# Optimization experiments

Measured on AMD Instinct MI355X. Metric: run time of the kernel, lower is better.

## Reference

```python
import jax, jax.numpy as jnp
import numpy as np

D = 768
H = 12
W = 128
HD = D // H
EPS = 1e-5


def setup_inputs() -> dict:
    key = jax.random.key(0)
    ks = jax.random.split(key, 10)
    B, L = 4, 8190
    s = 1.0 / np.sqrt(D)
    inp = {
        "expanded": jax.random.normal(ks[0], (B, L, D), dtype=jnp.float32),
        "Wq": jax.random.normal(ks[1], (D, D), dtype=jnp.float32) * s,
        "bq": jnp.zeros((D,), jnp.float32),
        "Wk": jax.random.normal(ks[2], (D, D), dtype=jnp.float32) * s,
        "bk": jnp.zeros((D,), jnp.float32),
        "Wv": jax.random.normal(ks[3], (D, D), dtype=jnp.float32) * s,
        "bv": jnp.zeros((D,), jnp.float32),
        "Wo": jax.random.normal(ks[4], (D, D), dtype=jnp.float32) * s,
        "bo": jnp.zeros((D,), jnp.float32),
        "ln_g": jnp.ones((D,), jnp.float32),
        "ln_b": jnp.zeros((D,), jnp.float32),
    }
    return inp


def _local_attn(x, Wq, bq, Wk, bk, Wv, bv, Wo, bo):
    # x: (B, Lp, D) with Lp % W == 0; block-local multihead attention per window
    B, Lp, _ = x.shape
    nW = Lp // W
    xw = x.reshape(B, nW, W, D)
    q = (xw @ Wq + bq).reshape(B, nW, W, H, HD)
    k = (xw @ Wk + bk).reshape(B, nW, W, H, HD)
    v = (xw @ Wv + bv).reshape(B, nW, W, H, HD)
    scale = 1.0 / jnp.sqrt(jnp.asarray(HD, x.dtype))
    # scores: (B, nW, H, W, W)
    scores = jnp.einsum("bnqhd,bnkhd->bnhqk", q, k) * scale
    p = jax.nn.softmax(scores, axis=-1)
    o = jnp.einsum("bnhqk,bnkhd->bnqhd", p, v).reshape(B, nW, W, D)
    o = o @ Wo + bo
    return o.reshape(B, Lp, D)


def reference(expanded, Wq, bq, Wk, bk, Wv, bv, Wo, bo, ln_g, ln_b):
    B, L, _ = expanded.shape
    pad_len = (W - L % W) % W
    x = jnp.pad(expanded, ((0, 0), (0, pad_len), (0, 0))) if pad_len > 0 else expanded
    attn = _local_attn(x, Wq, bq, Wk, bk, Wv, bv, Wo, bo)
    attn = attn[:, :L, :]
    y = expanded + attn
    mu = jnp.mean(y, axis=-1, keepdims=True)
    var = jnp.mean(jnp.square(y - mu), axis=-1, keepdims=True)
    return (y - mu) * jax.lax.rsqrt(var + EPS) * ln_g + ln_b
```

## Files before the change

### kernel.cpp

```cpp
#include <hip/hip_runtime.h>
#include <hip/hip_bf16.h>

#define D 768
#define NQKV 2304
#define NH 12
#define HD 64
#define BATCH 4
#define LSEQ 8190
#define LPAD 8192
#define TP (BATCH*LPAD)

typedef __bf16 bf16x8 __attribute__((ext_vector_type(8)));
typedef float f32x4 __attribute__((ext_vector_type(4)));
using bf16 = __hip_bfloat16;

__device__ __forceinline__ float b2f(bf16 x){ return __bfloat162float(x); }
__device__ __forceinline__ bf16 f2b(float x){ return __float2bfloat16(x); }
__device__ __forceinline__ f32x4 mfma16(bf16x8 a, bf16x8 b, f32x4 c){
    return __builtin_amdgcn_mfma_f32_16x16x32_bf16(a, b, c, 0, 0, 0);
}
__device__ __forceinline__ void gload_lds16(const void* g, void* l){
    __builtin_amdgcn_global_load_lds(
        (const __attribute__((address_space(1))) unsigned int*)g,
        (__attribute__((address_space(3))) unsigned int*)l, 16, 0, 0);
}

__global__ void k_transpose(const float* __restrict__ w0, const float* __restrict__ w1,
                            const float* __restrict__ w2, const float* __restrict__ w3,
                            bf16* __restrict__ WqkvT, bf16* __restrict__ WoT) {
    const float* src; bf16* dst;
    switch (blockIdx.y) {
        case 0:  src = w0; dst = WqkvT;               break;
        case 1:  src = w1; dst = WqkvT + D * D;       break;
        case 2:  src = w2; dst = WqkvT + 2 * D * D;   break;
        default: src = w3; dst = WoT;                 break;
    }
    int o = blockIdx.x * 256 + threadIdx.x;
    int n = o / D, k = o % D;
    dst[o] = f2b(src[k * D + n]);
}

__global__ __launch_bounds__(256) void k_prep(const float* __restrict__ X,
                                              bf16* __restrict__ Xb, int tok0)
{
    int idx = (blockIdx.x * 256 + threadIdx.x) * 8;
    int row = idx / D, col = idx % D;
    int gt = tok0 + row, b = gt >> 13, pos = gt & 8191;
    bf16 tmp[8];
    if (pos < LSEQ) {
        const float* s = &X[((size_t)b * LSEQ + pos) * D + col];
        float4 f0 = *reinterpret_cast<const float4*>(s);
        float4 f1 = *reinterpret_cast<const float4*>(s + 4);
        tmp[0]=f2b(f0.x); tmp[1]=f2b(f0.y); tmp[2]=f2b(f0.z); tmp[3]=f2b(f0.w);
        tmp[4]=f2b(f1.x); tmp[5]=f2b(f1.y); tmp[6]=f2b(f1.z); tmp[7]=f2b(f1.w);
    } else {
        #pragma unroll
        for (int j = 0; j < 8; ++j) tmp[j] = f2b(0.f);
    }
    *reinterpret_cast<uint4*>(&Xb[idx]) = *reinterpret_cast<const uint4*>(tmp);
}

__global__ __launch_bounds__(256) void k_gemm_qkv(
    const bf16* __restrict__ Xb, const bf16* __restrict__ Wt,
    const float* __restrict__ bq, const float* __restrict__ bk, const float* __restrict__ bv,
    bf16* __restrict__ Qkv)
{
    __shared__ bf16 a_lds[128 * 32];
    __shared__ bf16 b_lds[128 * 32];
    const int tid = threadIdx.x;
    const int rt = blockIdx.x, ct = blockIdx.y;
    const int wave = tid >> 6, lane = tid & 63, quad = lane >> 4, lm = lane & 15;
    const int wm = wave >> 1, wn = wave & 1;
    const int seg0 = wave * 2, seg1 = seg0 + 1;
    const int srow = lane >> 2, selem = (lane & 3) * 8;

    const bf16* Ag = Xb + (size_t)(rt * 128) * D;
    const bf16* Bg = Wt + (size_t)(ct * 128) * D;

    f32x4 acc[4][4] = {};

    for (int kt = 0; kt < D; kt += 32) {
        gload_lds16(Ag + (size_t)(seg0 * 16 + srow) * D + kt + selem, &a_lds[seg0 * 512]);
        gload_lds16(Ag + (size_t)(seg1 * 16 + srow) * D + kt + selem, &a_lds[seg1 * 512]);
        gload_lds16(Bg + (size_t)(seg0 * 16 + srow) * D + kt + selem, &b_lds[seg0 * 512]);
        gload_lds16(Bg + (size_t)(seg1 * 16 + srow) * D + kt + selem, &b_lds[seg1 * 512]);
        __syncthreads();
        bf16x8 af[4], bfr[4];
        #pragma unroll
        for (int i = 0; i < 4; ++i)
            af[i] = *reinterpret_cast<const bf16x8*>(&a_lds[(wm * 64 + i * 16 + lm) * 32 + quad * 8]);
        #pragma unroll
        for (int n = 0; n < 4; ++n)
            bfr[n] = *reinterpret_cast<const bf16x8*>(&b_lds[(wn * 64 + n * 16 + lm) * 32 + quad * 8]);
        #pragma unroll
        for (int i = 0; i < 4; ++i)
            #pragma unroll
            for (int n = 0; n < 4; ++n)
                acc[i][n] = mfma16(af[i], bfr[n], acc[i][n]);
        __syncthreads();
    }

    const float* bias = (ct < 6) ? bq : (ct < 12 ? bk : bv);
    const int cb = ct * 128 - (ct < 6 ? 0 : (ct < 12 ? D : 2 * D));
    float bvv[4];
    #pragma unroll
    for (int n = 0; n < 4; ++n)
        bvv[n] = bias[cb + wn * 64 + n * 16 + lm];

    #pragma unroll
    for (int i = 0; i < 4; ++i)
        #pragma unroll
        for (int reg = 0; reg < 4; ++reg) {
            int lrow = rt * 128 + wm * 64 + i * 16 + quad * 4 + reg;
            #pragma unroll
            for (int n = 0; n < 4; ++n) {
                int col = ct * 128 + wn * 64 + n * 16 + lm;
                Qkv[(size_t)lrow * NQKV + col] = f2b(acc[i][n][reg] + bvv[n]);
            }
        }
}

__global__ __launch_bounds__(256) void k_oproj(
    const bf16* __restrict__ Aq, const bf16* __restrict__ WoT,
    const float* __restrict__ bo, const float* __restrict__ X,
    float* __restrict__ out, int tok0)
{
    __shared__ bf16 a_lds[128 * 32];
    __shared__ bf16 b_lds[128 * 32];
    const int tid = threadIdx.x;
    const int rt = blockIdx.x, ct = blockIdx.y;
    const int wave = tid >> 6, lane = tid & 63, quad = lane >> 4, lm = lane & 15;
    const int wm = wave >> 1, wn = wave & 1;
    const int seg0 = wave * 2, seg1 = seg0 + 1;
    const int srow = lane >> 2, selem = (lane & 3) * 8;

    const bf16* Ag = Aq + (size_t)(rt * 128) * NQKV;
    const bf16* Bg = WoT + (size_t)(ct * 128) * D;

    f32x4 acc[4][4] = {};

    for (int kt = 0; kt < D; kt += 32) {
        gload_lds16(Ag + (size_t)(seg0 * 16 + srow) * NQKV + kt + selem, &a_lds[seg0 * 512]);
        gload_lds16(Ag + (size_t)(seg1 * 16 + srow) * NQKV + kt + selem, &a_lds[seg1 * 512]);
        gload_lds16(Bg + (size_t)(seg0 * 16 + srow) * D + kt + selem, &b_lds[seg0 * 512]);
        gload_lds16(Bg + (size_t)(seg1 * 16 + srow) * D + kt + selem, &b_lds[seg1 * 512]);
        __syncthreads();
        bf16x8 af[4], bfr[4];
        #pragma unroll
        for (int i = 0; i < 4; ++i)
            af[i] = *reinterpret_cast<const bf16x8*>(&a_lds[(wm * 64 + i * 16 + lm) * 32 + quad * 8]);
        #pragma unroll
        for (int n = 0; n < 4; ++n)
            bfr[n] = *reinterpret_cast<const bf16x8*>(&b_lds[(wn * 64 + n * 16 + lm) * 32 + quad * 8]);
        #pragma unroll
        for (int i = 0; i < 4; ++i)
            #pragma unroll
            for (int n = 0; n < 4; ++n)
                acc[i][n] = mfma16(af[i], bfr[n], acc[i][n]);
        __syncthreads();
    }

    float bvv[4];
    #pragma unroll
    for (int n = 0; n < 4; ++n)
        bvv[n] = bo[ct * 128 + wn * 64 + n * 16 + lm];

    #pragma unroll
    for (int i = 0; i < 4; ++i)
        #pragma unroll
        for (int reg = 0; reg < 4; ++reg) {
            int g = tok0 + rt * 128 + wm * 64 + i * 16 + quad * 4 + reg;
            int b = g >> 13, pos = g & 8191;
            if (pos >= LSEQ) continue;
            size_t orow = (size_t)b * LSEQ + pos;
            #pragma unroll
            for (int n = 0; n < 4; ++n) {
                int col = ct * 128 + wn * 64 + n * 16 + lm;
                out[orow * D + col] = acc[i][n][reg] + bvv[n] + X[orow * D + col];
            }
        }
}

__global__ __launch_bounds__(256) void k_attn(bf16* Qkv)
{
    __shared__ bf16 qk_lds[2 * 128 * 72];
    __shared__ bf16 vt_lds[64 * 136];
    const int tid = threadIdx.x;
    const int g0 = blockIdx.x * 128, hc = blockIdx.y * 64;
    const int wave = tid >> 6, lane = tid & 63, quad = lane >> 4, lm = lane & 15;
    const int wq = wave * 32;
    bf16* Q_lds = qk_lds;
    bf16* K_lds = qk_lds + 128 * 72;
    bf16* P_lds = qk_lds;

    #pragma unroll
    for (int p = 0; p < 4; ++p) {
        int cid = tid + p * 256;
        int r = cid >> 3, cc = (cid & 7) * 8;
        size_t rb = (size_t)(g0 + r) * NQKV;
        *reinterpret_cast<uint4*>(&Q_lds[r * 72 + cc]) =
            *reinterpret_cast<const uint4*>(&Qkv[rb + hc + cc]);
        *reinterpret_cast<uint4*>(&K_lds[r * 72 + cc]) =
            *reinterpret_cast<const uint4*>(&Qkv[rb + D + hc + cc]);
        uint4 vv = *reinterpret_cast<const uint4*>(&Qkv[rb + 2 * D + hc + cc]);
        const bf16* ve = reinterpret_cast<const bf16*>(&vv);
        #pragma unroll
        for (int j = 0; j < 8; ++j) vt_lds[(cc + j) * 136 + r] = ve[j];
    }
    __syncthreads();

    f32x4 s[2][8] = {};
    #pragma unroll
    for (int ks = 0; ks < HD; ks += 32) {
        bf16x8 aq[2];
        #pragma unroll
        for (int i = 0; i < 2; ++i)
            aq[i] = *reinterpret_cast<const bf16x8*>(&Q_lds[(wq + i * 16 + lm) * 72 + ks + quad * 8]);
        #pragma unroll
        for (int nt = 0; nt < 8; ++nt) {
            bf16x8 bk = *reinterpret_cast<const bf16x8*>(&K_lds[(nt * 16 + lm) * 72 + ks + quad * 8]);
            s[0][nt] = mfma16(aq[0], bk, s[0][nt]);
            s[1][nt] = mfma16(aq[1], bk, s[1][nt]);
        }
    }
    __syncthreads();

    const float scale = 0.125f;
    #pragma unroll
    for (int i = 0; i < 2; ++i)
        #pragma unroll
        for (int reg = 0; reg < 4; ++reg) {
            float m = -1e30f;
            #pragma unroll
            for (int nt = 0; nt < 8; ++nt) m = fmaxf(m, s[i][nt][reg]);
            #pragma unroll
            for (int off = 8; off >= 1; off >>= 1) m = fmaxf(m, __shfl_xor(m, off));
            float pv[8]; float sum = 0.f;
            #pragma unroll
            for (int nt = 0; nt < 8; ++nt) {
                float p = __expf((s[i][nt][reg] - m) * scale);
                pv[nt] = p; sum += p;
            }
            #pragma unroll
            for (int off = 8; off >= 1; off >>= 1) sum += __shfl_xor(sum, off);
            float rinv = 1.f / sum;
            int row = wq + i * 16 + quad * 4 + reg;
            #pragma unroll
            for (int nt = 0; nt < 8; ++nt)
                P_lds[row * 136 + nt * 16 + lm] = f2b(pv[nt] * rinv);
        }
    __syncthreads();

    f32x4 o[2][4] = {};
    #pragma unroll
    for (int ks = 0; ks < 128; ks += 32) {
        bf16x8 ap[2];
        #pragma unroll
        for (int i = 0; i < 2; ++i)
            ap[i] = *reinterpret_cast<const bf16x8*>(&P_lds[(wq + i * 16 + lm) * 136 + ks + quad * 8]);
        #pragma unroll
        for (int n = 0; n < 4; ++n) {
            bf16x8 bv = *reinterpret_cast<const bf16x8*>(&vt_lds[(n * 16 + lm) * 136 + ks + quad * 8]);
            o[0][n] = mfma16(ap[0], bv, o[0][n]);
            o[1][n] = mfma16(ap[1], bv, o[1][n]);
        }
    }
    #pragma unroll
    for (int i = 0; i < 2; ++i)
        #pragma unroll
        for (int reg = 0; reg < 4; ++reg) {
            int row = wq + i * 16 + quad * 4 + reg;
            #pragma unroll
            for (int n = 0; n < 4; ++n)
                Qkv[(size_t)(g0 + row) * NQKV + hc + n * 16 + lm] = f2b(o[i][n][reg]);
        }
}

__global__ __launch_bounds__(256) void k_ln(const float* __restrict__ g_,
                                            const float* __restrict__ b_,
                                            float* __restrict__ y)
{
    __shared__ float red[256];
    const size_t base = (size_t)blockIdx.x * D;
    const int tid = threadIdx.x;
    float v[3];
    #pragma unroll
    for (int j = 0; j < 3; ++j) v[j] = y[base + tid + j * 256];

    red[tid] = v[0] + v[1] + v[2];
    __syncthreads();
    for (int o = 128; o > 0; o >>= 1) {
        if (tid < o) red[tid] += red[tid + o];
        __syncthreads();
    }
    float mu = red[0] * (1.f / 768.f);
    __syncthreads();

    float d0 = v[0] - mu, d1 = v[1] - mu, d2 = v[2] - mu;
    red[tid] = d0 * d0 + d1 * d1 + d2 * d2;
    __syncthreads();
    for (int o = 128; o > 0; o >>= 1) {
        if (tid < o) red[tid] += red[tid + o];
        __syncthreads();
    }
    float var = red[0] * (1.f / 768.f);
    float r = rsqrtf(var + 1e-5f);

    #pragma unroll
    for (int j = 0; j < 3; ++j) {
        int c = tid + j * 256;
        y[base + c] = (v[j] - mu) * r * g_[c] + b_[c];
    }
}

extern "C" void kernel_launch(void* const* d_in, const int* in_sizes, int n_in,
                              void* d_out, int out_size, void* d_ws, size_t ws_size,
                              hipStream_t stream)
{
    const float* expanded = (const float*)d_in[0];
    const float* Wq = (const float*)d_in[1];
    const float* bq = (const float*)d_in[2];
    const float* Wk = (const float*)d_in[3];
    const float* bk = (const float*)d_in[4];
    const float* Wv = (const float*)d_in[5];
    const float* bv = (const float*)d_in[6];
    const float* Wo = (const float*)d_in[7];
    const float* bo = (const float*)d_in[8];
    const float* ln_g = (const float*)d_in[9];
    const float* ln_b = (const float*)d_in[10];
    float* out = (float*)d_out;

    char* ws = (char*)d_ws;
    const size_t WSZ = (size_t)D * D * sizeof(bf16);
    bf16* WqkvT = (bf16*)(ws);
    bf16* WoT   = (bf16*)(ws + 3 * WSZ);
    const size_t fixed = 4 * WSZ;

    int cht = TP;
    while (cht > 128 && fixed + (size_t)cht * (D + NQKV) * sizeof(bf16) > ws_size)
        cht >>= 1;
    bf16* Xb  = (bf16*)(ws + fixed);
    bf16* Qkv = (bf16*)(ws + fixed + (size_t)cht * D * sizeof(bf16));

    k_transpose<<<dim3((D * D) / 256, 4), 256, 0, stream>>>(Wq, Wk, Wv, Wo, WqkvT, WoT);

    for (int t0 = 0; t0 < TP; t0 += cht) {
        k_prep<<<(cht * D) / 2048, 256, 0, stream>>>(expanded, Xb, t0);
        k_gemm_qkv<<<dim3(cht / 128, NQKV / 128), 256, 0, stream>>>(
            Xb, WqkvT, bq, bk, bv, Qkv);
        k_attn<<<dim3(cht / 128, NH), 256, 0, stream>>>(Qkv);
        k_oproj<<<dim3(cht / 128, D / 128), 256, 0, stream>>>(
            Qkv, WoT, bo, expanded, out, t0);
    }

    k_ln<<<BATCH * LSEQ, 256, 0, stream>>>(ln_g, ln_b, out);
}
```

Baseline: 533.6 us.

## Rewrite QKV GEMM with 256x256 tiles, 4-stage LDS pipeline and swizzle

```diff
diff --git a/kernel.cpp b/kernel.cpp
--- a/kernel.cpp
+++ b/kernel.cpp
@@ -60,63 +60,120 @@
     *reinterpret_cast<uint4*>(&Xb[idx]) = *reinterpret_cast<const uint4*>(tmp);
 }
 
-__global__ __launch_bounds__(256) void k_gemm_qkv(
+__global__ __launch_bounds__(512, 2) void k_gemm_qkv(
     const bf16* __restrict__ Xb, const bf16* __restrict__ Wt,
     const float* __restrict__ bq, const float* __restrict__ bk, const float* __restrict__ bv,
     bf16* __restrict__ Qkv)
 {
-    __shared__ bf16 a_lds[128 * 32];
-    __shared__ bf16 b_lds[128 * 32];
+    __shared__ alignas(16) bf16 a_lds[4 * 8192];
+    __shared__ alignas(16) bf16 b_lds[4 * 8192];
+
     const int tid = threadIdx.x;
-    const int rt = blockIdx.x, ct = blockIdx.y;
     const int wave = tid >> 6, lane = tid & 63, quad = lane >> 4, lm = lane & 15;
-    const int wm = wave >> 1, wn = wave & 1;
-    const int seg0 = wave * 2, seg1 = seg0 + 1;
-    const int srow = lane >> 2, selem = (lane & 3) * 8;
-
-    const bf16* Ag = Xb + (size_t)(rt * 128) * D;
-    const bf16* Bg = Wt + (size_t)(ct * 128) * D;
-
-    f32x4 acc[4][4] = {};
-
-    for (int kt = 0; kt < D; kt += 32) {
-        gload_lds16(Ag + (size_t)(seg0 * 16 + srow) * D + kt + selem, &a_lds[seg0 * 512]);
-        gload_lds16(Ag + (size_t)(seg1 * 16 + srow) * D + kt + selem, &a_lds[seg1 * 512]);
-        gload_lds16(Bg + (size_t)(seg0 * 16 + srow) * D + kt + selem, &b_lds[seg0 * 512]);
-        gload_lds16(Bg + (size_t)(seg1 * 16 + srow) * D + kt + selem, &b_lds[seg1 * 512]);
-        __syncthreads();
+    const int wm = wave >> 2, wn = wave & 3;
+
+    int bid = blockIdx.x;
+    const int nwg = gridDim.x;
+    if ((nwg & 7) == 0) { const int cpx = nwg >> 3; bid = (bid & 7) * cpx + (bid >> 3); }
+    const int rt = bid / 9, ct = bid % 9;
+
+    const int r_loc = tid >> 2;
+    const int swslot = ((tid & 3) ^ ((r_loc >> 1) & 3)) * 8;
+    const bf16* a_src = Xb + (size_t)(rt * 256 + r_loc) * D + swslot;
+    const bf16* b_src = Wt + (size_t)(ct * 256 + r_loc) * D + swslot;
+    const int dA = wave * 512;
+
+    #pragma unroll
+    for (int pt = 0; pt < 3; ++pt) {
+        bf16* ab = a_lds + pt * 8192;
+        bf16* bb = b_lds + pt * 8192;
+        const int ko = pt * 32;
+        gload_lds16(a_src + ko,           ab + dA);
+        gload_lds16(a_src + 128 * D + ko, ab + 4096 + dA);
+        gload_lds16(b_src + ko,           bb + dA);
+        gload_lds16(b_src + 128 * D + ko, bb + 4096 + dA);
+    }
+    asm volatile("s_waitcnt vmcnt(8)" ::: "memory");
+    __builtin_amdgcn_s_barrier();
+
+    const int sw = (quad ^ ((lm >> 1) & 3)) * 8;
+    const int aoff = (wm * 128 + lm) * 32 + sw;
+    const int boff = (wn * 64 + lm) * 32 + sw;
+
+    f32x4 acc[8][4] = {};
+
+    #pragma unroll 1
+    for (int t = 0; t < 24; ++t) {
+        const bf16* ab = a_lds + (t & 3) * 8192;
+        const bf16* bb = b_lds + (t & 3) * 8192;
+
         bf16x8 af[4], bfr[4];
         #pragma unroll
         for (int i = 0; i < 4; ++i)
-            af[i] = *reinterpret_cast<const bf16x8*>(&a_lds[(wm * 64 + i * 16 + lm) * 32 + quad * 8]);
+            af[i] = *reinterpret_cast<const bf16x8*>(&ab[aoff + i * 512]);
         #pragma unroll
         for (int n = 0; n < 4; ++n)
-            bfr[n] = *reinterpret_cast<const bf16x8*>(&b_lds[(wn * 64 + n * 16 + lm) * 32 + quad * 8]);
+            bfr[n] = *reinterpret_cast<const bf16x8*>(&bb[boff + n * 512]);
+        if (t < 21) {
+            bf16* abn = a_lds + ((t + 3) & 3) * 8192;
+            const int ko = (t + 3) * 32;
+            gload_lds16(a_src + ko,           abn + dA);
+            gload_lds16(a_src + 128 * D + ko, abn + 4096 + dA);
+        }
+        __builtin_amdgcn_s_barrier();
+        __builtin_amdgcn_s_setprio(1);
         #pragma unroll
         for (int i = 0; i < 4; ++i)
             #pragma unroll
             for (int n = 0; n < 4; ++n)
                 acc[i][n] = mfma16(af[i], bfr[n], acc[i][n]);
-        __syncthreads();
-    }
-
-    const float* bias = (ct < 6) ? bq : (ct < 12 ? bk : bv);
-    const int cb = ct * 128 - (ct < 6 ? 0 : (ct < 12 ? D : 2 * D));
+        __builtin_amdgcn_s_setprio(0);
+        __builtin_amdgcn_s_barrier();
+
+        bf16x8 ag[4];
+        #pragma unroll
+        for (int i = 0; i < 4; ++i)
+            ag[i] = *reinterpret_cast<const bf16x8*>(&ab[aoff + (i + 4) * 512]);
+        if (t < 21) {
+            bf16* bbn = b_lds + ((t + 3) & 3) * 8192;
+            const int ko = (t + 3) * 32;
+            gload_lds16(b_src + ko,           bbn + dA);
+            gload_lds16(b_src + 128 * D + ko, bbn + 4096 + dA);
+        }
+        __builtin_amdgcn_s_barrier();
+        __builtin_amdgcn_s_setprio(1);
+        #pragma unroll
+        for (int i = 0; i < 4; ++i)
+            #pragma unroll
+            for (int n = 0; n < 4; ++n)
+                acc[i + 4][n] = mfma16(ag[i], bfr[n], acc[i + 4][n]);
+        __builtin_amdgcn_s_setprio(0);
+
+        if (t <= 20)      asm volatile("s_waitcnt vmcnt(8)" ::: "memory");
+        else if (t == 21) asm volatile("s_waitcnt vmcnt(4)" ::: "memory");
+        else if (t == 22) asm volatile("s_waitcnt vmcnt(0)" ::: "memory");
+        if (t < 23) __builtin_amdgcn_s_barrier();
+    }
+
+    const float* bias; int cb;
+    if (ct < 3)      { bias = bq; cb = ct * 256; }
+    else if (ct < 6) { bias = bk; cb = ct * 256 - D; }
+    else             { bias = bv; cb = ct * 256 - 2 * D; }
     float bvv[4];
     #pragma unroll
     for (int n = 0; n < 4; ++n)
         bvv[n] = bias[cb + wn * 64 + n * 16 + lm];
 
-    #pragma unroll
-    for (int i = 0; i < 4; ++i)
+    const int row0 = rt * 256 + wm * 128 + quad * 4;
+    const int col0 = ct * 256 + wn * 64 + lm;
+    #pragma unroll
+    for (int i = 0; i < 8; ++i)
         #pragma unroll
         for (int reg = 0; reg < 4; ++reg) {
-            int lrow = rt * 128 + wm * 64 + i * 16 + quad * 4 + reg;
-            #pragma unroll
-            for (int n = 0; n < 4; ++n) {
-                int col = ct * 128 + wn * 64 + n * 16 + lm;
-                Qkv[(size_t)lrow * NQKV + col] = f2b(acc[i][n][reg] + bvv[n]);
-            }
+            size_t r = (size_t)(row0 + i * 16 + reg) * NQKV;
+            #pragma unroll
+            for (int n = 0; n < 4; ++n)
+                Qkv[r + col0 + n * 16] = f2b(acc[i][n][reg] + bvv[n]);
         }
 }
 
@@ -337,7 +394,7 @@
     const size_t fixed = 4 * WSZ;
 
     int cht = TP;
-    while (cht > 128 && fixed + (size_t)cht * (D + NQKV) * sizeof(bf16) > ws_size)
+    while (cht > 256 && fixed + (size_t)cht * (D + NQKV) * sizeof(bf16) > ws_size)
         cht >>= 1;
     bf16* Xb  = (bf16*)(ws + fixed);
     bf16* Qkv = (bf16*)(ws + fixed + (size_t)cht * D * sizeof(bf16));
@@ -346,7 +403,7 @@
 
     for (int t0 = 0; t0 < TP; t0 += cht) {
         k_prep<<<(cht * D) / 2048, 256, 0, stream>>>(expanded, Xb, t0);
-        k_gemm_qkv<<<dim3(cht / 128, NQKV / 128), 256, 0, stream>>>(
+        k_gemm_qkv<<<dim3((cht / 256) * 9), 512, 0, stream>>>(
             Xb, WqkvT, bq, bk, bv, Qkv);
         k_attn<<<dim3(cht / 128, NH), 256, 0, stream>>>(Qkv);
         k_oproj<<<dim3(cht / 128, D / 128), 256, 0, stream>>>(
```

Result: no change. 523.9 us (-1.8%).
